# Optimization experiments

Measured on AMD Instinct MI355X. Metric: run time of the kernel, lower is better.

The kernel has to match this reference:

```python
import jax, jax.numpy as jnp
import numpy as np

C = 51  # num_relation


def setup_inputs() -> dict:
    key = jax.random.key(0)
    N_o, N_u, D = 16384, 16384, 1024
    k = jax.random.split(key, 6)
    feat = jax.random.normal(k[0], (N_o + N_u, D), jnp.float32)
    # first N_o rows are labeled (label != 0), remaining N_u rows unlabeled (label == 0)
    label = jnp.concatenate([
        jax.random.randint(k[1], (N_o,), 1, C),
        jnp.zeros((N_u,), jnp.int32),
    ]).astype(jnp.int32)
    W_o = jax.random.normal(k[2], (C, D), jnp.float32) * 0.03
    b_o = jnp.zeros((C,), jnp.float32)
    W = jax.random.normal(k[3], (C, D), jnp.float32) * 0.03
    b = jnp.zeros((C,), jnp.float32)
    cls = jnp.arange(C)
    group_mid_mask = (cls >= 16) & (cls < 36)   # groups[1]
    group_tail_mask = cls >= 36                 # groups[2]
    # runtime torch.randint partner sampling, hoisted to input construction
    idx_m = jax.random.randint(k[4], (2, N_u), 0, N_o)  # 2 mid copies
    idx_t = jax.random.randint(k[5], (3, N_u), 0, N_o)  # 3 tail copies
    return dict(feat=feat, label=label, W_o=W_o, b_o=b_o, W=W, b=b,
                group_mid_mask=group_mid_mask, group_tail_mask=group_tail_mask,
                idx_m=idx_m, idx_t=idx_t)


def reference(feat, label, W_o, b_o, W, b, group_mid_mask, group_tail_mask, idx_m, idx_t):
    n_u = idx_m.shape[1]
    n_o = feat.shape[0] - n_u
    feat_o, feat_u = feat[:n_o], feat[n_o:]
    label_o = label[:n_o]

    # fc_o under no_grad, then softmax / top-1 rank + score
    logits = jax.lax.stop_gradient(feat_u @ W_o.T + b_o)      # [N_u, C]
    p = jax.nn.softmax(logits, axis=1)
    pred = jnp.argmax(p, axis=1)                               # ranks[:,0]
    score = jnp.max(p, axis=1)                                 # score[:,0]

    # group membership + confidence thresholds (heads are unused in the original)
    mid_m = group_mid_mask[pred] & (score > 0.5)
    tail_m = group_tail_mask[pred] & (score > 0.3)

    oh_u = jax.nn.one_hot(pred, C, dtype=feat.dtype)
    oh_o = jax.nn.one_hot(label_o, C, dtype=feat.dtype)

    im = idx_m.reshape(-1)   # [2*N_u]
    it = idx_t.reshape(-1)   # [3*N_u]

    fm = 0.7 * feat_o[im] + 0.3 * jnp.tile(feat_u, (2, 1))
    lm = 0.7 * oh_o[im] + 0.3 * jnp.tile(oh_u, (2, 1))
    ft = 0.7 * feat_o[it] + 0.3 * jnp.tile(feat_u, (3, 1))
    lt = 0.7 * oh_o[it] + 0.3 * jnp.tile(oh_u, (3, 1))

    feat_cat = jnp.concatenate([fm, ft], axis=0)               # [5*N_u, D]
    label_cat = jnp.concatenate([lm, lt], axis=0)              # [5*N_u, C]
    w = jnp.concatenate([jnp.tile(mid_m, 2), jnp.tile(tail_m, 3)]).astype(feat.dtype)

    # soft-label cross entropy on fc(feat_cat); masked mean over selected rows
    logp = jax.nn.log_softmax(feat_cat @ W.T + b, axis=1)
    ce = -(logp * label_cat).sum(axis=1)
    cnt = w.sum()
    return (ce * w).sum() / jnp.maximum(cnt, 1.0)
```

## Files before the change

### kernel.cpp

```cpp
#include <hip/hip_runtime.h>
#include <math.h>

#define DD 1024
#define NU 16384
#define NO 16384
#define NCEB 256

typedef short short8 __attribute__((ext_vector_type(8)));
typedef float f32x4 __attribute__((ext_vector_type(4)));

__device__ __forceinline__ unsigned short f2b(float x) {
    unsigned int u = __float_as_uint(x);
    u += 0x7FFFu + ((u >> 16) & 1u);
    return (unsigned short)(u >> 16);
}

__device__ __forceinline__ short8 cvt8(float4 a, float4 b) {
    short8 r;
    r[0] = (short)f2b(a.x); r[1] = (short)f2b(a.y);
    r[2] = (short)f2b(a.z); r[3] = (short)f2b(a.w);
    r[4] = (short)f2b(b.x); r[5] = (short)f2b(b.y);
    r[6] = (short)f2b(b.z); r[7] = (short)f2b(b.w);
    return r;
}

__device__ __forceinline__ void gl_lds(const void* g, void* l) {
    __builtin_amdgcn_global_load_lds(
        (const __attribute__((address_space(1))) void*)g,
        (__attribute__((address_space(3))) void*)l, 16, 0, 0);
}

__global__ __launch_bounds__(256) void convW(const float* __restrict__ W_o,
                                             unsigned short* __restrict__ Wcat,
                                             int* __restrict__ cnt,
                                             double* __restrict__ gnum,
                                             int* __restrict__ gcnt,
                                             int* __restrict__ gdone) {
    if (blockIdx.x == 0 && threadIdx.x == 0) {
        cnt[0] = 0; gnum[0] = 0.0; gcnt[0] = 0; gdone[0] = 0;
    }
    const int n = blockIdx.x;
    const int k = threadIdx.x * 4;
    const float* src = (n < 51) ? (W_o + (size_t)n * DD) : nullptr;
    float4 v = src ? *(const float4*)(src + k) : make_float4(0.f, 0.f, 0.f, 0.f);
    ushort4 o;
    o.x = f2b(v.x); o.y = f2b(v.y); o.z = f2b(v.z); o.w = f2b(v.w);
    *(ushort4*)(Wcat + (size_t)n * DD + k) = o;
}

__global__ __launch_bounds__(256, 4) void gemm_u(const float* __restrict__ feat,
                                                 const unsigned short* __restrict__ Wcat,
                                                 const float* __restrict__ b_o,
                                                 const int* __restrict__ idxm,
                                                 const int* __restrict__ idxt,
                                                 int* __restrict__ cnt,
                                                 int2* __restrict__ list) {
    __shared__ __attribute__((aligned(16))) char lds[3 * 12288];
    const int m0 = blockIdx.x * 64;
    const int tid = threadIdx.x;
    const int lane = tid & 63;
    const int w = tid >> 6;
    const int m = lane & 15;
    const int quad = lane >> 4;
    const int s = m & 7;
    const int s2 = m & 3;

    const char *gs0, *gs1, *gs2;
    int lo0, lo1, lo2;
    { const int r = w * 16 + (lane >> 3);
      const int g = (lane & 7) ^ (r & 7);
      gs0 = (const char*)(feat + (size_t)(NO + m0 + r) * DD + g * 4); lo0 = (w * 2) * 1024; }
    { const int r = w * 16 + 8 + (lane >> 3);
      const int g = (lane & 7) ^ (r & 7);
      gs1 = (const char*)(feat + (size_t)(NO + m0 + r) * DD + g * 4); lo1 = (w * 2 + 1) * 1024; }
    { const int r = w * 16 + (lane >> 2);
      const int g = (lane & 3) ^ (r & 3);
      gs2 = (const char*)(Wcat + (size_t)r * DD + g * 8); lo2 = 8192 + w * 1024; }

    f32x4 acc[4];
#pragma unroll
    for (int nf = 0; nf < 4; ++nf) acc[nf] = (f32x4){0.f, 0.f, 0.f, 0.f};

    const int rA = w * 16 + m;

#define STAGE(t, buf)                                  \
    do {                                               \
        gl_lds(gs0 + (size_t)(t) * 128, (buf) + lo0);  \
        gl_lds(gs1 + (size_t)(t) * 128, (buf) + lo1);  \
        gl_lds(gs2 + (size_t)(t) * 64,  (buf) + lo2);  \
    } while (0)

    STAGE(0, lds);
    STAGE(1, lds + 12288);

    int bc = 0;
    for (int kt = 0; kt < 32; ++kt) {
        if (kt < 30) {
            const int bi2 = (bc == 0) ? 2 : bc - 1;
            STAGE(kt + 2, lds + bi2 * 12288);
            asm volatile("s_waitcnt vmcnt(6)\n\ts_barrier" ::: "memory");
        } else if (kt == 30) {
            asm volatile("s_waitcnt vmcnt(3)\n\ts_barrier" ::: "memory");
        } else {
            asm volatile("s_waitcnt vmcnt(0)\n\ts_barrier" ::: "memory");
        }
        const char* buf = lds + bc * 12288;
        const float4 f0 = *(const float4*)(buf + rA * 128 + ((2 * quad) ^ s) * 16);
        const float4 f1 = *(const float4*)(buf + rA * 128 + ((2 * quad + 1) ^ s) * 16);
        const short8 af = cvt8(f0, f1);
#pragma unroll
        for (int nf = 0; nf < 4; ++nf) {
            const short8 bf =
                *(const short8*)(buf + 8192 + (m + nf * 16) * 64 + (quad ^ s2) * 16);
            acc[nf] = __builtin_amdgcn_mfma_f32_16x16x32_bf16(af, bf, acc[nf], 0, 0, 0);
        }
        bc = (bc == 2) ? 0 : bc + 1;
    }
#undef STAGE

    const int rloc = m0 + w * 16 + quad * 4;
    float boc[4];
#pragma unroll
    for (int c = 0; c < 4; ++c) {
        const int col = c * 16 + m;
        boc[c] = (col < 51) ? b_o[col] : 0.f;
    }
#pragma unroll
    for (int r = 0; r < 4; ++r) {
        float z[4];
        float mx = acc[0][r] + boc[0];
        int mi = m;
        z[0] = mx;
#pragma unroll
        for (int c = 1; c < 4; ++c) {
            const int col = c * 16 + m;
            z[c] = (col < 51) ? acc[c][r] + boc[c] : -INFINITY;
            if (z[c] > mx) { mx = z[c]; mi = col; }
        }
#pragma unroll
        for (int off = 1; off < 16; off <<= 1) {
            const float om = __shfl_xor(mx, off);
            const int oi = __shfl_xor(mi, off);
            if (om > mx || (om == mx && oi < mi)) { mx = om; mi = oi; }
        }
        float e = 0.f;
#pragma unroll
        for (int c = 0; c < 4; ++c)
            if (c * 16 + m < 51) e += expf(z[c] - mx);
#pragma unroll
        for (int off = 1; off < 16; off <<= 1) e += __shfl_xor(e, off);
        const float score = 1.f / e;
        const int mid = (mi >= 16 && mi < 36 && score > 0.5f) ? 1 : 0;
        const int tail = (mi >= 36 && score > 0.3f) ? 1 : 0;
        const int nref = mid ? 2 : (tail ? 3 : 0);
        if (m < nref) {
            const int u = rloc + r;
            const int oo = mid ? idxm[(size_t)m * NU + u]
                               : idxt[(size_t)m * NU + u];
            const int p = atomicAdd(cnt, 1);
            list[p] = make_int2(oo, u | (mi << 16));
        }
    }
}

__global__ __launch_bounds__(256) void cekernel(const float* __restrict__ feat,
                                                const float* __restrict__ W,
                                                const float* __restrict__ bb,
                                                const int* __restrict__ label,
                                                const int* __restrict__ cnt,
                                                const int2* __restrict__ list,
                                                double* __restrict__ gnum,
                                                int* __restrict__ gcnt,
                                                int* __restrict__ gdone,
                                                float* __restrict__ out) {
    __shared__ float snum[4];
    __shared__ int scnt[4];
    const int w = threadIdx.x >> 6;
    const int lane = threadIdx.x & 63;
    const int n = cnt[0];
    const float bbv = (lane < 51) ? bb[lane] : 0.f;
    float fsum = 0.f;
    int ccnt = 0;
    for (int t = blockIdx.x * 4 + w; t < n; t += NCEB * 4) {
        const int2 e = list[t];
        const int ob = e.x;
        const int ub = e.y & 0xFFFF;
        const int pu = e.y >> 16;
        const f32x4* fo4 = (const f32x4*)(feat + (size_t)ob * DD);
        const f32x4* fu4 = (const f32x4*)(feat + (size_t)(NO + ub) * DD);
        f32x4 g[4];
#pragma unroll
        for (int q = 0; q < 4; ++q)
            g[q] = 0.7f * fo4[q * 64 + lane] + 0.3f * fu4[q * 64 + lane];
        float zmy = 0.f;
        for (int c = 0; c < 51; ++c) {
            const f32x4* wr = (const f32x4*)(W + (size_t)c * DD);
            f32x4 p = wr[lane] * g[0];
            p += wr[64 + lane] * g[1];
            p += wr[128 + lane] * g[2];
            p += wr[192 + lane] * g[3];
            float d = (p[0] + p[1]) + (p[2] + p[3]);
#pragma unroll
            for (int off = 1; off < 64; off <<= 1) d += __shfl_xor(d, off);
            if (lane == c) zmy = d;
        }
        const float z = (lane < 51) ? zmy + bbv : -INFINITY;
        float mx = z;
#pragma unroll
        for (int off = 1; off < 64; off <<= 1) mx = fmaxf(mx, __shfl_xor(mx, off));
        float e2 = (lane < 51) ? expf(z - mx) : 0.f;
#pragma unroll
        for (int off = 1; off < 64; off <<= 1) e2 += __shfl_xor(e2, off);
        const float lse = mx + logf(e2);
        const int lo = label[ob];
        const float zlo = __shfl(z, lo);
        const float zpu = __shfl(z, pu);
        fsum += lse - 0.7f * zlo - 0.3f * zpu;
        ++ccnt;
    }
    if (lane == 0) { snum[w] = fsum; scnt[w] = ccnt; }
    __syncthreads();
    if (threadIdx.x == 0) {
        const float bn = snum[0] + snum[1] + snum[2] + snum[3];
        const int bcnt = scnt[0] + scnt[1] + scnt[2] + scnt[3];
        if (bcnt > 0) {
            atomicAdd(gnum, (double)bn);
            atomicAdd(gcnt, bcnt);
        }
        __threadfence();
        const int dn = atomicAdd(gdone, 1);
        if (dn == NCEB - 1) {
            const double nn = atomicAdd(gnum, 0.0);
            const int cc = atomicAdd(gcnt, 0);
            out[0] = (float)(nn / (cc > 1 ? (double)cc : 1.0));
        }
    }
}

extern "C" void kernel_launch(void* const* d_in, const int* in_sizes, int n_in,
                              void* d_out, int out_size, void* d_ws, size_t ws_size,
                              hipStream_t stream) {
    const float* feat = (const float*)d_in[0];
    const int* label = (const int*)d_in[1];
    const float* W_o = (const float*)d_in[2];
    const float* b_o = (const float*)d_in[3];
    const float* W = (const float*)d_in[4];
    const float* b = (const float*)d_in[5];
    const int* idxm = (const int*)d_in[8];
    const int* idxt = (const int*)d_in[9];

    char* ws = (char*)d_ws;
    unsigned short* Wcat = (unsigned short*)ws;
    int* cntp = (int*)(ws + 131072);
    double* gnum = (double*)(ws + 131088);
    int* gcnt = (int*)(ws + 131096);
    int* gdone = (int*)(ws + 131100);
    int2* list = (int2*)(ws + 131104);

    convW<<<64, 256, 0, stream>>>(W_o, Wcat, cntp, gnum, gcnt, gdone);
    gemm_u<<<256, 256, 0, stream>>>(feat, Wcat, b_o, idxm, idxt, cntp, list);
    cekernel<<<NCEB, 256, 0, stream>>>(feat, W, b, label, cntp, list,
                                       gnum, gcnt, gdone, (float*)d_out);
}
```

Measured before the change: 231.8 us.

## Fuse pseudo-label GEMM and CE into one kernel with per-block list

Measured after the change: 226.4 us. 2.3% less time.

```diff
diff --git a/kernel.cpp b/kernel.cpp
--- a/kernel.cpp
+++ b/kernel.cpp
@@ -4,7 +4,6 @@
 #define DD 1024
 #define NU 16384
 #define NO 16384
-#define NCEB 256
 
 typedef short short8 __attribute__((ext_vector_type(8)));
 typedef float f32x4 __attribute__((ext_vector_type(4)));
@@ -30,32 +29,22 @@
         (__attribute__((address_space(3))) void*)l, 16, 0, 0);
 }
 
-__global__ __launch_bounds__(256) void convW(const float* __restrict__ W_o,
-                                             unsigned short* __restrict__ Wcat,
-                                             int* __restrict__ cnt,
-                                             double* __restrict__ gnum,
-                                             int* __restrict__ gcnt,
-                                             int* __restrict__ gdone) {
-    if (blockIdx.x == 0 && threadIdx.x == 0) {
-        cnt[0] = 0; gnum[0] = 0.0; gcnt[0] = 0; gdone[0] = 0;
-    }
-    const int n = blockIdx.x;
-    const int k = threadIdx.x * 4;
-    const float* src = (n < 51) ? (W_o + (size_t)n * DD) : nullptr;
-    float4 v = src ? *(const float4*)(src + k) : make_float4(0.f, 0.f, 0.f, 0.f);
-    ushort4 o;
-    o.x = f2b(v.x); o.y = f2b(v.y); o.z = f2b(v.z); o.w = f2b(v.w);
-    *(ushort4*)(Wcat + (size_t)n * DD + k) = o;
-}
-
-__global__ __launch_bounds__(256, 4) void gemm_u(const float* __restrict__ feat,
-                                                 const unsigned short* __restrict__ Wcat,
-                                                 const float* __restrict__ b_o,
-                                                 const int* __restrict__ idxm,
-                                                 const int* __restrict__ idxt,
-                                                 int* __restrict__ cnt,
-                                                 int2* __restrict__ list) {
-    __shared__ __attribute__((aligned(16))) char lds[3 * 12288];
+__global__ __launch_bounds__(256) void fused(const float* __restrict__ feat,
+                                             const float* __restrict__ W_o,
+                                             const float* __restrict__ b_o,
+                                             const float* __restrict__ W,
+                                             const float* __restrict__ bb,
+                                             const int* __restrict__ label,
+                                             const int* __restrict__ idxm,
+                                             const int* __restrict__ idxt,
+                                             double* __restrict__ pnum,
+                                             int* __restrict__ pcnt) {
+    __shared__ __attribute__((aligned(16))) char lds[3 * 16384];
+    __shared__ int2 slist[192];
+    __shared__ int scount;
+    __shared__ float swsum[4];
+    __shared__ int swcnt[4];
+
     const int m0 = blockIdx.x * 64;
     const int tid = threadIdx.x;
     const int lane = tid & 63;
@@ -63,19 +52,26 @@
     const int m = lane & 15;
     const int quad = lane >> 4;
     const int s = m & 7;
-    const int s2 = m & 3;
-
-    const char *gs0, *gs1, *gs2;
-    int lo0, lo1, lo2;
+
+    if (tid == 0) scount = 0;
+    __syncthreads();
+
+    const char *gs0, *gs1, *gs2, *gs3;
+    int lo0, lo1, lo2, lo3;
     { const int r = w * 16 + (lane >> 3);
       const int g = (lane & 7) ^ (r & 7);
       gs0 = (const char*)(feat + (size_t)(NO + m0 + r) * DD + g * 4); lo0 = (w * 2) * 1024; }
     { const int r = w * 16 + 8 + (lane >> 3);
       const int g = (lane & 7) ^ (r & 7);
       gs1 = (const char*)(feat + (size_t)(NO + m0 + r) * DD + g * 4); lo1 = (w * 2 + 1) * 1024; }
-    { const int r = w * 16 + (lane >> 2);
-      const int g = (lane & 3) ^ (r & 3);
-      gs2 = (const char*)(Wcat + (size_t)r * DD + g * 8); lo2 = 8192 + w * 1024; }
+    { const int r = w * 16 + (lane >> 3);
+      const int rc = (r > 50) ? 50 : r;
+      const int g = (lane & 7) ^ (r & 7);
+      gs2 = (const char*)(W_o + (size_t)rc * DD + g * 4); lo2 = 8192 + (w * 2) * 1024; }
+    { const int r = w * 16 + 8 + (lane >> 3);
+      const int rc = (r > 50) ? 50 : r;
+      const int g = (lane & 7) ^ (r & 7);
+      gs3 = (const char*)(W_o + (size_t)rc * DD + g * 4); lo3 = 8192 + (w * 2 + 1) * 1024; }
 
     f32x4 acc[4];
 #pragma unroll
@@ -87,31 +83,34 @@
     do {                                               \
         gl_lds(gs0 + (size_t)(t) * 128, (buf) + lo0);  \
         gl_lds(gs1 + (size_t)(t) * 128, (buf) + lo1);  \
-        gl_lds(gs2 + (size_t)(t) * 64,  (buf) + lo2);  \
+        gl_lds(gs2 + (size_t)(t) * 128, (buf) + lo2);  \
+        gl_lds(gs3 + (size_t)(t) * 128, (buf) + lo3);  \
     } while (0)
 
     STAGE(0, lds);
-    STAGE(1, lds + 12288);
+    STAGE(1, lds + 16384);
 
     int bc = 0;
     for (int kt = 0; kt < 32; ++kt) {
         if (kt < 30) {
             const int bi2 = (bc == 0) ? 2 : bc - 1;
-            STAGE(kt + 2, lds + bi2 * 12288);
-            asm volatile("s_waitcnt vmcnt(6)\n\ts_barrier" ::: "memory");
+            STAGE(kt + 2, lds + bi2 * 16384);
+            asm volatile("s_waitcnt vmcnt(8)\n\ts_barrier" ::: "memory");
         } else if (kt == 30) {
-            asm volatile("s_waitcnt vmcnt(3)\n\ts_barrier" ::: "memory");
+            asm volatile("s_waitcnt vmcnt(4)\n\ts_barrier" ::: "memory");
         } else {
             asm volatile("s_waitcnt vmcnt(0)\n\ts_barrier" ::: "memory");
         }
-        const char* buf = lds + bc * 12288;
+        const char* buf = lds + bc * 16384;
         const float4 f0 = *(const float4*)(buf + rA * 128 + ((2 * quad) ^ s) * 16);
         const float4 f1 = *(const float4*)(buf + rA * 128 + ((2 * quad + 1) ^ s) * 16);
         const short8 af = cvt8(f0, f1);
 #pragma unroll
         for (int nf = 0; nf < 4; ++nf) {
-            const short8 bf =
-                *(const short8*)(buf + 8192 + (m + nf * 16) * 64 + (quad ^ s2) * 16);
+            const int row = m + nf * 16;
+            const float4 b0 = *(const float4*)(buf + 8192 + row * 128 + ((2 * quad) ^ s) * 16);
+            const float4 b1 = *(const float4*)(buf + 8192 + row * 128 + ((2 * quad + 1) ^ s) * 16);
+            const short8 bf = cvt8(b0, b1);
             acc[nf] = __builtin_amdgcn_mfma_f32_16x16x32_bf16(af, bf, acc[nf], 0, 0, 0);
         }
         bc = (bc == 2) ? 0 : bc + 1;
@@ -157,32 +156,18 @@
             const int u = rloc + r;
             const int oo = mid ? idxm[(size_t)m * NU + u]
                                : idxt[(size_t)m * NU + u];
-            const int p = atomicAdd(cnt, 1);
-            list[p] = make_int2(oo, u | (mi << 16));
-        }
-    }
-}
-
-__global__ __launch_bounds__(256) void cekernel(const float* __restrict__ feat,
-                                                const float* __restrict__ W,
-                                                const float* __restrict__ bb,
-                                                const int* __restrict__ label,
-                                                const int* __restrict__ cnt,
-                                                const int2* __restrict__ list,
-                                                double* __restrict__ gnum,
-                                                int* __restrict__ gcnt,
-                                                int* __restrict__ gdone,
-                                                float* __restrict__ out) {
-    __shared__ float snum[4];
-    __shared__ int scnt[4];
-    const int w = threadIdx.x >> 6;
-    const int lane = threadIdx.x & 63;
-    const int n = cnt[0];
+            const int p = atomicAdd(&scount, 1);
+            slist[p] = make_int2(oo, u | (mi << 16));
+        }
+    }
+    __syncthreads();
+
+    const int n = scount;
     const float bbv = (lane < 51) ? bb[lane] : 0.f;
     float fsum = 0.f;
     int ccnt = 0;
-    for (int t = blockIdx.x * 4 + w; t < n; t += NCEB * 4) {
-        const int2 e = list[t];
+    for (int t = w; t < n; t += 4) {
+        const int2 e = slist[t];
         const int ob = e.x;
         const int ub = e.y & 0xFFFF;
         const int pu = e.y >> 16;
@@ -218,22 +203,35 @@
         fsum += lse - 0.7f * zlo - 0.3f * zpu;
         ++ccnt;
     }
-    if (lane == 0) { snum[w] = fsum; scnt[w] = ccnt; }
+    if (lane == 0) { swsum[w] = fsum; swcnt[w] = ccnt; }
+    __syncthreads();
+    if (tid == 0) {
+        pnum[blockIdx.x] = (double)swsum[0] + (double)swsum[1] +
+                           (double)swsum[2] + (double)swsum[3];
+        pcnt[blockIdx.x] = swcnt[0] + swcnt[1] + swcnt[2] + swcnt[3];
+    }
+}
+
+__global__ __launch_bounds__(256) void finalize(const double* __restrict__ pnum,
+                                                const int* __restrict__ pcnt,
+                                                float* __restrict__ out) {
+    __shared__ double sd[4];
+    __shared__ int sc[4];
+    const int w = threadIdx.x >> 6;
+    const int lane = threadIdx.x & 63;
+    double s = pnum[threadIdx.x];
+    int c = pcnt[threadIdx.x];
+#pragma unroll
+    for (int off = 1; off < 64; off <<= 1) {
+        s += __shfl_xor(s, off);
+        c += __shfl_xor(c, off);
+    }
+    if (lane == 0) { sd[w] = s; sc[w] = c; }
     __syncthreads();
     if (threadIdx.x == 0) {
-        const float bn = snum[0] + snum[1] + snum[2] + snum[3];
-        const int bcnt = scnt[0] + scnt[1] + scnt[2] + scnt[3];
-        if (bcnt > 0) {
-            atomicAdd(gnum, (double)bn);
-            atomicAdd(gcnt, bcnt);
-        }
-        __threadfence();
-        const int dn = atomicAdd(gdone, 1);
-        if (dn == NCEB - 1) {
-            const double nn = atomicAdd(gnum, 0.0);
-            const int cc = atomicAdd(gcnt, 0);
-            out[0] = (float)(nn / (cc > 1 ? (double)cc : 1.0));
-        }
+        const double n = sd[0] + sd[1] + sd[2] + sd[3];
+        const int cc = sc[0] + sc[1] + sc[2] + sc[3];
+        out[0] = (float)(n / (cc > 1 ? (double)cc : 1.0));
     }
 }
 
@@ -250,15 +248,10 @@
     const int* idxt = (const int*)d_in[9];
 
     char* ws = (char*)d_ws;
-    unsigned short* Wcat = (unsigned short*)ws;
-    int* cntp = (int*)(ws + 131072);
-    double* gnum = (double*)(ws + 131088);
-    int* gcnt = (int*)(ws + 131096);
-    int* gdone = (int*)(ws + 131100);
-    int2* list = (int2*)(ws + 131104);
-
-    convW<<<64, 256, 0, stream>>>(W_o, Wcat, cntp, gnum, gcnt, gdone);
-    gemm_u<<<256, 256, 0, stream>>>(feat, Wcat, b_o, idxm, idxt, cntp, list);
-    cekernel<<<NCEB, 256, 0, stream>>>(feat, W, b, label, cntp, list,
-                                       gnum, gcnt, gdone, (float*)d_out);
-}
+    double* pnum = (double*)ws;
+    int* pcnt = (int*)(ws + 2048);
+
+    fused<<<256, 256, 0, stream>>>(feat, W_o, b_o, W, b, label, idxm, idxt,
+                                   pnum, pcnt);
+    finalize<<<1, 256, 0, stream>>>(pnum, pcnt, (float*)d_out);
+}
```
